# Performance work log

Measured on AMD Instinct MI355X. Metric: run time of the kernel, lower is better.

The kernel has to match this reference:

```python
import math
import jax, jax.numpy as jnp
import numpy as np

S, D = 4096, 2048
H, DH = 16, 128
ROPE_BASE = 10000.0


def _rotate_half(x):
    # x: [..., dh]; pairs (x1, x2) -> (-x2, x1), interleaved
    shp = x.shape
    x = x.reshape(*shp[:-1], shp[-1] // 2, 2)
    x1, x2 = x[..., 0], x[..., 1]
    return jnp.stack((-x2, x1), axis=-1).reshape(shp)


def _rope_cos_sin(seq_len, dh):
    inv_freq = 1.0 / (ROPE_BASE ** (jnp.arange(0, dh, 2, dtype=jnp.float32) / dh))
    t = jnp.arange(seq_len, dtype=jnp.float32)
    freqs = jnp.einsum('i,j->ij', t, inv_freq)  # [S, dh/2]
    cos = jnp.repeat(jnp.cos(freqs), 2, axis=-1)  # [S, dh]
    sin = jnp.repeat(jnp.sin(freqs), 2, axis=-1)
    return cos, sin


def setup_inputs() -> dict:
    key = jax.random.key(0)
    kx, kq, kk, kv, ko = jax.random.split(key, 5)
    scale_in = 1.0 / math.sqrt(D)
    scale_hd = 1.0 / math.sqrt(H * DH)
    return {
        'x': jax.random.normal(kx, (S, D), dtype=jnp.float32),
        'mask': jnp.tril(jnp.ones((S, S), dtype=bool)),  # causal
        'wq': jax.random.normal(kq, (H * DH, D), dtype=jnp.float32) * scale_in,
        'wk': jax.random.normal(kk, (H * DH, D), dtype=jnp.float32) * scale_in,
        'wv': jax.random.normal(kv, (H * DH, D), dtype=jnp.float32) * scale_in,
        'wo': jax.random.normal(ko, (D, H * DH), dtype=jnp.float32) * scale_hd,
    }


def reference(x, mask, wq, wk, wv, wo):
    s = x.shape[0]
    # QKV projections (Linear: y = W @ x per token) -> [h, S, dh]
    q = (x @ wq.T).reshape(s, H, DH).transpose(1, 0, 2)
    k = (x @ wk.T).reshape(s, H, DH).transpose(1, 0, 2)
    v = (x @ wv.T).reshape(s, H, DH).transpose(1, 0, 2)
    # RoPE
    cos, sin = _rope_cos_sin(s, DH)  # [S, dh] each
    q = q * cos[None] + _rotate_half(q) * sin[None]
    k = k * cos[None] + _rotate_half(k) * sin[None]
    # Attention
    sim = jnp.einsum('hid,hjd->hij', q, k) / math.sqrt(DH)  # [h, S, S]
    sim = jnp.where(mask[None], sim, -jnp.inf)
    attn = jax.nn.softmax(sim, axis=-1)
    out = jnp.einsum('hij,hjd->ihd', attn, v).reshape(s, H * DH)
    return out @ wo.T
```

## Files before the change

### kernel.cpp

```cpp
#include <hip/hip_runtime.h>
#include <stdint.h>

#define S_LEN 4096
#define D_MODEL 2048
#define NH 16
#define DH 128

typedef short s16x8 __attribute__((ext_vector_type(8)));
typedef short s16x2 __attribute__((ext_vector_type(2)));
typedef unsigned short u16;
typedef unsigned short u16x4 __attribute__((ext_vector_type(4)));
typedef float f32x4 __attribute__((ext_vector_type(4)));

__device__ __forceinline__ u16 f2bf(float f) {
  union { float f; uint32_t u; } v; v.f = f;
  uint32_t u = v.u;
  u += 0x7FFFu + ((u >> 16) & 1u);
  return (u16)(u >> 16);
}

__device__ __forceinline__ float bf2f(u16 b) {
  union { uint32_t u; float f; } v; v.u = ((uint32_t)b) << 16;
  return v.f;
}

__device__ __forceinline__ void async_copy16(const u16* g, u16* l) {
  __builtin_amdgcn_global_load_lds(
      (const __attribute__((address_space(1))) unsigned int*)g,
      (__attribute__((address_space(3))) unsigned int*)l, 16, 0, 0);
}

__global__ void cast_kernel(const float4* __restrict__ src, u16* __restrict__ dst, int n4) {
  int i = blockIdx.x * blockDim.x + threadIdx.x;
  if (i >= n4) return;
  float4 v = src[i];
  u16x4 o;
  o[0] = f2bf(v.x); o[1] = f2bf(v.y); o[2] = f2bf(v.z); o[3] = f2bf(v.w);
  *(u16x4*)(dst + (size_t)i * 4) = o;
}

__global__ void cast4_kernel(const float4* __restrict__ s0, const float4* __restrict__ s1,
                             const float4* __restrict__ s2, const float4* __restrict__ s3,
                             u16* __restrict__ d0, u16* __restrict__ d1,
                             u16* __restrict__ d2, u16* __restrict__ d3) {
  int b = blockIdx.x;
  int which = b >> 12;
  const float4* src = which == 0 ? s0 : which == 1 ? s1 : which == 2 ? s2 : s3;
  u16* dst = which == 0 ? d0 : which == 1 ? d1 : which == 2 ? d2 : d3;
  int i = (b & 4095) * blockDim.x + threadIdx.x;
  float4 v = src[i];
  u16x4 o;
  o[0] = f2bf(v.x); o[1] = f2bf(v.y); o[2] = f2bf(v.z); o[3] = f2bf(v.w);
  *(u16x4*)(dst + (size_t)i * 4) = o;
}

__global__ void rope_table(float* __restrict__ ctab, float* __restrict__ stab) {
  int idx = blockIdx.x * blockDim.x + threadIdx.x;
  int t = idx >> 6, p = idx & 63;
  float invf = powf(10000.0f, -(float)p / 64.0f);
  float th = (float)t * invf;
  ctab[idx] = cosf(th);
  stab[idx] = sinf(th);
}

#define G256_BAR() __builtin_amdgcn_s_barrier()
#define G256_LGK0() do { asm volatile("s_waitcnt lgkmcnt(0)" ::: "memory"); \
                         __builtin_amdgcn_sched_barrier(0); } while (0)
#define G256_VMC4() asm volatile("s_waitcnt vmcnt(4)" ::: "memory")

__device__ __forceinline__ void stage128(const u16* __restrict__ src, u16* dst,
                                         int rr, int gc, int ldk) {
  const u16* s = src + (size_t)rr * ldk + gc;
  u16* d = dst + (threadIdx.x << 3);
  async_copy16(s, d);
  async_copy16(s + (size_t)64 * ldk, d + 4096);
}

__device__ __forceinline__ void mma256_core(
    const u16* __restrict__ Ab,
    const u16* __restrict__ Bb,
    const int K, u16* lds, f32x4 (&acc)[8][4])
{
  const int tid = threadIdx.x;
  const int lane = tid & 63, quad = lane >> 4, l16 = lane & 15;
  const int w = tid >> 6, wr = w >> 2, wc = w & 3;
  const int rr = tid >> 3;
  const int gc = ((tid & 7) ^ (rr & 7)) << 3;

  u16* const A0b = lds;
  u16* const B0b = lds + 16384;
  u16* const A1b = lds + 32768;
  u16* const B1b = lds + 49152;

  const int NT = K >> 6;

  auto sA = [&](int t, int hh, u16* buf) {
    int tc = t < NT ? t : NT - 1;
    stage128(Ab + (size_t)(hh << 7) * K + ((size_t)tc << 6), buf + (hh << 13), rr, gc, K);
  };
  auto sB = [&](int t, int hh, u16* buf) {
    int tc = t < NT ? t : NT - 1;
    stage128(Bb + (size_t)(hh << 7) * K + ((size_t)tc << 6), buf + (hh << 13), rr, gc, K);
  };

  s16x8 a[4][2], b[4][2];
  auto rA = [&](const u16* buf, int mh) {
#pragma unroll
    for (int mt = 0; mt < 4; ++mt) {
      int ra = (wr << 7) + (mh << 6) + (mt << 4) + l16;
#pragma unroll
      for (int ks = 0; ks < 2; ++ks)
        a[mt][ks] = *(const s16x8*)(buf + (ra << 6) + ((((ks << 2) + quad) ^ (ra & 7)) << 3));
    }
  };
  auto rB = [&](const u16* buf, int nh) {
#pragma unroll
    for (int nt = 0; nt < 2; ++nt) {
      int rb = (wc << 6) + (((nh << 1) + nt) << 4) + l16;
#pragma unroll
      for (int ks = 0; ks < 2; ++ks)
        b[(nh << 1) + nt][ks] =
            *(const s16x8*)(buf + (rb << 6) + ((((ks << 2) + quad) ^ (rb & 7)) << 3));
    }
  };
  auto mmaq = [&](int mh, int nh) {
    __builtin_amdgcn_s_setprio(1);
#pragma unroll
    for (int mt = 0; mt < 4; ++mt)
#pragma unroll
      for (int nt = 0; nt < 2; ++nt) {
#pragma unroll
        for (int ks = 0; ks < 2; ++ks)
          acc[(mh << 2) + mt][(nh << 1) + nt] = __builtin_amdgcn_mfma_f32_16x16x32_bf16(
              a[mt][ks], b[(nh << 1) + nt][ks], acc[(mh << 2) + mt][(nh << 1) + nt], 0, 0, 0);
      }
    __builtin_amdgcn_s_setprio(0);
  };

  sB(0, 0, B0b); sB(0, 1, B0b); sA(0, 0, A0b); sA(0, 1, A0b);
  sB(1, 0, B1b); sB(1, 1, B1b);
  G256_VMC4();
  G256_BAR();

  const int NI = K >> 7;
#pragma unroll 1
  for (int i = 0; i < NI; ++i) {
    const int t1 = 2 * i + 1, t2 = 2 * i + 2, t3 = 2 * i + 3;
    sA(t1, 0, A1b);
    rA(A0b, 0); rB(B0b, 0);
    G256_BAR(); G256_LGK0(); mmaq(0, 0); G256_BAR();
    sA(t1, 1, A1b);
    rB(B0b, 1);
    G256_BAR(); G256_LGK0(); mmaq(0, 1); G256_BAR();
    sB(t2, 0, B0b);
    rA(A0b, 1);
    G256_BAR(); G256_LGK0(); mmaq(1, 0); G256_BAR();
    sB(t2, 1, B0b);
    G256_VMC4();
    G256_BAR(); mmaq(1, 1); G256_BAR();
    sA(t2, 0, A0b);
    rA(A1b, 0); rB(B1b, 0);
    G256_BAR(); G256_LGK0(); mmaq(0, 0); G256_BAR();
    sA(t2, 1, A0b);
    rB(B1b, 1);
    G256_BAR(); G256_LGK0(); mmaq(0, 1); G256_BAR();
    sB(t3, 0, B1b);
    rA(A1b, 1);
    G256_BAR(); G256_LGK0(); mmaq(1, 0); G256_BAR();
    sB(t3, 1, B1b);
    G256_VMC4();
    G256_BAR(); mmaq(1, 1); G256_BAR();
  }
}

__global__ __launch_bounds__(512) void gemm256_qkv(
    const u16* __restrict__ A,
    const u16* __restrict__ wqb, const u16* __restrict__ wkb, const u16* __restrict__ wvb,
    u16* __restrict__ qh, u16* __restrict__ kh, u16* __restrict__ vh,
    const float* __restrict__ ctab, const float* __restrict__ stab)
{
  __shared__ __align__(16) u16 lds[65536];
  const int tid = threadIdx.x;
  const int lane = tid & 63, quad = lane >> 4, l16 = lane & 15;
  const int w = tid >> 6, wr = w >> 2, wc = w & 3;
  const int m0 = blockIdx.x << 8;
  const int by = blockIdx.y;
  const int which = by >> 3;
  const int n0 = (by & 7) << 8;
  const u16* B = which == 0 ? wqb : which == 1 ? wkb : wvb;
  u16* outp = which == 0 ? qh : which == 1 ? kh : vh;

  f32x4 acc[8][4];
  f32x4 zero = {0.f, 0.f, 0.f, 0.f};
#pragma unroll
  for (int i = 0; i < 8; ++i)
#pragma unroll
    for (int j = 0; j < 4; ++j) acc[i][j] = zero;

  mma256_core(A + (size_t)m0 * D_MODEL, B + (size_t)n0 * D_MODEL, D_MODEL, lds, acc);

#pragma unroll
  for (int Mt = 0; Mt < 8; ++Mt) {
    int rowg = m0 + (wr << 7) + (Mt << 4) + (quad << 2);
#pragma unroll
    for (int Nt = 0; Nt < 4; ++Nt) {
      int cl = n0 + (wc << 6) + (Nt << 4) + l16;
      int hh = cl >> 7, dd = cl & 127;
      int p = dd >> 1;
      f32x4 v = acc[Mt][Nt];
#pragma unroll
      for (int r = 0; r < 4; ++r) {
        float val = v[r];
        if (which < 2) {
          float partner = __shfl_xor(val, 1);
          float c = ctab[(size_t)(rowg + r) * 64 + p];
          float s = stab[(size_t)(rowg + r) * 64 + p];
          val = (dd & 1) ? fmaf(val, c, partner * s) : fmaf(val, c, -partner * s);
        }
        outp[((size_t)hh * S_LEN + (rowg + r)) * DH + dd] = f2bf(val);
      }
    }
  }
}

__global__ __launch_bounds__(512) void gemm256_out(
    const u16* __restrict__ A, const u16* __restrict__ B, float* __restrict__ outF)
{
  __shared__ __align__(16) u16 lds[65536];
  const int tid = threadIdx.x;
  const int lane = tid & 63, quad = lane >> 4, l16 = lane & 15;
  const int w = tid >> 6, wr = w >> 2, wc = w & 3;
  const int m0 = blockIdx.x << 8, n0 = blockIdx.y << 8;

  f32x4 acc[8][4];
  f32x4 zero = {0.f, 0.f, 0.f, 0.f};
#pragma unroll
  for (int i = 0; i < 8; ++i)
#pragma unroll
    for (int j = 0; j < 4; ++j) acc[i][j] = zero;

  mma256_core(A + (size_t)m0 * D_MODEL, B + (size_t)n0 * D_MODEL, D_MODEL, lds, acc);

#pragma unroll
  for (int Mt = 0; Mt < 8; ++Mt) {
    int rowg = m0 + (wr << 7) + (Mt << 4) + (quad << 2);
#pragma unroll
    for (int Nt = 0; Nt < 4; ++Nt) {
      int col = n0 + (wc << 6) + (Nt << 4) + l16;
      f32x4 v = acc[Mt][Nt];
#pragma unroll
      for (int r = 0; r < 4; ++r) outF[(size_t)(rowg + r) * D_MODEL + col] = v[r];
    }
  }
}

__global__ __launch_bounds__(512) void attn_kernel(
    const u16* __restrict__ Q, const u16* __restrict__ Kb,
    const u16* __restrict__ V,
    u16* __restrict__ U0, u16* __restrict__ U1, float* __restrict__ lbuf)
{
  __shared__ __align__(16) u16 lk[2][64 * 128];
  __shared__ __align__(16) u16 lvt[2][128 * 64];
  __shared__ __align__(16) u16 lp[8 * 1024];

  const int tid = threadIdx.x;
  const int w = tid >> 6, lane = tid & 63, quad = lane >> 4, l16 = lane & 15;
  const int h = blockIdx.y;
  const int bx = blockIdx.x;

  const u16* Qh = Q + (size_t)h * S_LEN * DH;
  const u16* Kh = Kb + (size_t)h * S_LEN * DH;
  const u16* Vh = V + (size_t)h * S_LEN * DH;

  const float scale = 0.08838834764831845f;
  const s16x8 vones = {0x3F80, 0x3F80, 0x3F80, 0x3F80, 0x3F80, 0x3F80, 0x3F80, 0x3F80};
  f32x4 zero = {0.f, 0.f, 0.f, 0.f};
  u16* lpw = lp + (w << 10);

  for (int seg = 0; seg < 2; ++seg) {
    const int qt = seg ? bx : (31 - bx);
    const int jlo = seg ? (qt + 1) : 0;
    const int jhi = seg ? (2 * qt + 2) : (qt + 1);
    const int i0 = qt << 7;
    const int iw = i0 + (w << 4);

    s16x8 qf[4];
#pragma unroll
    for (int ks = 0; ks < 4; ++ks)
      qf[ks] = *(const s16x8*)(Qh + (size_t)(iw + l16) * DH + ks * 32 + quad * 8);

    f32x4 accO[8];
#pragma unroll
    for (int dt = 0; dt < 8; ++dt) accO[dt] = zero;
    f32x4 accL = zero;

    {
      const int j0 = jlo << 6;
      int u = tid & 31, c8 = tid >> 5, r0 = u << 1;
      s16x8 v0 = *(const s16x8*)(Vh + (size_t)(j0 + r0) * DH + (c8 << 3));
      s16x8 v1 = *(const s16x8*)(Vh + (size_t)(j0 + r0 + 1) * DH + (c8 << 3));
#pragma unroll
      for (int rnd = 0; rnd < 2; ++rnd) {
        int c = rnd * 512 + tid;
        int r = c >> 4, cc = c & 15;
        int gcol = ((cc ^ (r & 15)) << 3);
        async_copy16(Kh + (size_t)(j0 + r) * DH + gcol, lk[0] + ((rnd * 512 + w * 64) << 3));
      }
      int cc = r0 >> 3;
#pragma unroll
      for (int e = 0; e < 8; ++e) {
        int d = (c8 << 3) + e;
        int off = (d << 6) + ((cc ^ (d & 7)) << 3) + (r0 & 7);
        s16x2 pr = {v0[e], v1[e]};
        *(s16x2*)(lvt[0] + off) = pr;
      }
    }
    __syncthreads();

    int cur = 0;
    for (int jt = jlo; jt < jhi; ++jt) {
      const int j0 = jt << 6;
      const bool has_next = (jt + 1) < jhi;

      s16x8 nv0, nv1;
      if (has_next) {
        const int nj0 = (jt + 1) << 6;
        int u = tid & 31, c8 = tid >> 5, r0 = u << 1;
        nv0 = *(const s16x8*)(Vh + (size_t)(nj0 + r0) * DH + (c8 << 3));
        nv1 = *(const s16x8*)(Vh + (size_t)(nj0 + r0 + 1) * DH + (c8 << 3));
#pragma unroll
        for (int rnd = 0; rnd < 2; ++rnd) {
          int c = rnd * 512 + tid;
          int r = c >> 4, cc = c & 15;
          int gcol = ((cc ^ (r & 15)) << 3);
          async_copy16(Kh + (size_t)(nj0 + r) * DH + gcol,
                       lk[cur ^ 1] + ((rnd * 512 + w * 64) << 3));
        }
      }

      const u16* lkc = lk[cur];
      f32x4 sa[4];
#pragma unroll
      for (int nt = 0; nt < 4; ++nt) sa[nt] = zero;
      __builtin_amdgcn_s_setprio(1);
#pragma unroll
      for (int ks = 0; ks < 4; ++ks) {
#pragma unroll
        for (int nt = 0; nt < 4; ++nt) {
          int row = (nt << 4) + l16;
          s16x8 kf = *(const s16x8*)(lkc + (row << 7) + ((((ks << 2) + quad) ^ (row & 15)) << 3));
          sa[nt] = __builtin_amdgcn_mfma_f32_16x16x32_bf16(qf[ks], kf, sa[nt], 0, 0, 0);
        }
      }
      __builtin_amdgcn_s_setprio(0);

      const bool maskt = (j0 + 63 > iw);
#pragma unroll
      for (int nt = 0; nt < 4; ++nt) {
        int col = (nt << 4) + l16;
        int j = j0 + col;
        int ccp = col >> 3;
#pragma unroll
        for (int r = 0; r < 4; ++r) {
          float raw = sa[nt][r];
          if (maskt) {
            int i = iw + (quad << 2) + r;
            if (j > i) raw = -1.0e30f;
          }
          float p = __expf(fmaf(raw, scale, -8.0f));
          union { float f; uint32_t u; } pv; pv.f = p;
          int m = (quad << 2) + r;
          lpw[(m << 6) + ((ccp ^ (m & 7)) << 3) + (col & 7)] = (u16)(pv.u >> 16);
        }
      }
      asm volatile("s_waitcnt lgkmcnt(0)" ::: "memory");
      s16x8 pf[2];
#pragma unroll
      for (int kp = 0; kp < 2; ++kp)
        pf[kp] = *(const s16x8*)(lpw + (l16 << 6) + ((((kp << 2) + quad) ^ (l16 & 7)) << 3));

      if (has_next) {
        int u = tid & 31, c8 = tid >> 5, r0 = u << 1;
        int cc = r0 >> 3;
        u16* dst = lvt[cur ^ 1];
#pragma unroll
        for (int e = 0; e < 8; ++e) {
          int d = (c8 << 3) + e;
          int off = (d << 6) + ((cc ^ (d & 7)) << 3) + (r0 & 7);
          s16x2 pr = {nv0[e], nv1[e]};
          *(s16x2*)(dst + off) = pr;
        }
      }

      const u16* lvc = lvt[cur];
      __builtin_amdgcn_s_setprio(1);
      accL = __builtin_amdgcn_mfma_f32_16x16x32_bf16(pf[0], vones, accL, 0, 0, 0);
      accL = __builtin_amdgcn_mfma_f32_16x16x32_bf16(pf[1], vones, accL, 0, 0, 0);
#pragma unroll
      for (int dt = 0; dt < 8; ++dt) {
#pragma unroll
        for (int kp = 0; kp < 2; ++kp) {
          int row = (dt << 4) + l16;
          s16x8 vf = *(const s16x8*)(lvc + (row << 6) + ((((kp << 2) + quad) ^ (row & 7)) << 3));
          accO[dt] = __builtin_amdgcn_mfma_f32_16x16x32_bf16(pf[kp], vf, accO[dt], 0, 0, 0);
        }
      }
      __builtin_amdgcn_s_setprio(0);

      __syncthreads();
      cur ^= 1;
    }

    u16* Useg = seg ? U1 : U0;
    float* ls = lbuf + (size_t)seg * NH * S_LEN + (size_t)h * S_LEN;
#pragma unroll
    for (int r = 0; r < 4; ++r) {
      float lr = accL[r];
      float inv = lr > 0.f ? 1.0f / lr : 0.f;
      int srow = iw + (quad << 2) + r;
#pragma unroll
      for (int dt = 0; dt < 8; ++dt)
        Useg[((size_t)h * S_LEN + srow) * DH + (dt << 4) + l16] = f2bf(accO[dt][r] * inv);
      if (l16 == 0) ls[srow] = lr;
    }
  }
}

__global__ void combine_kernel(const u16* __restrict__ U0, const u16* __restrict__ U1,
                               const float* __restrict__ lbuf, u16* __restrict__ ob)
{
  int t = blockIdx.x * 256 + threadIdx.x;
  int d8 = t & 15;
  int h = (t >> 4) & 15;
  int s = t >> 8;
  float l0 = lbuf[(size_t)h * S_LEN + s];
  float l1 = lbuf[(size_t)(NH * S_LEN) + (size_t)h * S_LEN + s];
  float inv = 1.0f / (l0 + l1);
  float w0 = l0 * inv, w1 = l1 * inv;
  size_t base = ((size_t)h * S_LEN + s) * DH + d8 * 8;
  s16x8 u0 = *(const s16x8*)(U0 + base);
  s16x8 u1 = *(const s16x8*)(U1 + base);
  u16 o[8];
#pragma unroll
  for (int e = 0; e < 8; ++e)
    o[e] = f2bf(w0 * bf2f((u16)u0[e]) + w1 * bf2f((u16)u1[e]));
  *(s16x8*)(ob + ((size_t)s * D_MODEL + h * DH + d8 * 8)) = *(s16x8*)o;
}

extern "C" void kernel_launch(void* const* d_in, const int* in_sizes, int n_in,
                              void* d_out, int out_size, void* d_ws, size_t ws_size,
                              hipStream_t stream) {
  const float* x  = (const float*)d_in[0];
  const float* wq = (const float*)d_in[2];
  const float* wk = (const float*)d_in[3];
  const float* wv = (const float*)d_in[4];
  const float* wo = (const float*)d_in[5];
  float* out = (float*)d_out;

  char* ws = (char*)d_ws;
  u16* xb  = (u16*)(ws);
  u16* wqb = (u16*)(ws + (16ull << 20));
  u16* wkb = (u16*)(ws + (24ull << 20));
  u16* wvb = (u16*)(ws + (32ull << 20));
  u16* wob = (u16*)(ws + (40ull << 20));
  u16* qh  = (u16*)(ws + (48ull << 20));
  u16* kh  = (u16*)(ws + (64ull << 20));
  u16* vh  = (u16*)(ws + (80ull << 20));
  float* ctab = (float*)(ws + (96ull << 20));
  float* stab = (float*)(ws + (97ull << 20));
  u16* U0 = (u16*)(ws);
  u16* U1 = (u16*)(ws + (16ull << 20));
  float* lbuf = (float*)(ws + (32ull << 20));
  u16* ob = qh;

  const int nx4 = S_LEN * D_MODEL / 4;
  cast_kernel<<<nx4 / 256, 256, 0, stream>>>((const float4*)x, xb, nx4);
  cast4_kernel<<<4 * 4096, 256, 0, stream>>>(
      (const float4*)wq, (const float4*)wk, (const float4*)wv, (const float4*)wo,
      wqb, wkb, wvb, wob);
  rope_table<<<(S_LEN * 64) / 256, 256, 0, stream>>>(ctab, stab);

  gemm256_qkv<<<dim3(S_LEN / 256, 3 * D_MODEL / 256), 512, 0, stream>>>(
      xb, wqb, wkb, wvb, qh, kh, vh, ctab, stab);

  attn_kernel<<<dim3(32, NH), 512, 0, stream>>>(qh, kh, vh, U0, U1, lbuf);
  combine_kernel<<<S_LEN * NH * 16 / 256, 256, 0, stream>>>(U0, U1, lbuf, ob);

  gemm256_out<<<dim3(S_LEN / 256, D_MODEL / 256), 512, 0, stream>>>(
      ob, wob, out);
}
```

Measured before the change: 510.8 us.

## Switch projection GEMMs to 256x128 tiles with register double-buffered ping-pong schedule

Both the QKV and output projection GEMMs now use 256x128 output tiles instead of 256x256, with an 8-wave 4x2 layout and 96 KB of LDS instead of 128 KB. The main loop is restructured so that fragments for the next K-tile are loaded into a second register set while the current MFMAs run, with global staging issued mid-phase. The grid doubles, which improves wave quantization and may let more blocks fit per CU. The cost is lower arithmetic intensity per tile, more redundant A loads, and extra barriers.

```diff
diff --git a/kernel.cpp b/kernel.cpp
--- a/kernel.cpp
+++ b/kernel.cpp
@@ -63,113 +63,114 @@
   stab[idx] = sinf(th);
 }
 
-#define G256_BAR() __builtin_amdgcn_s_barrier()
-#define G256_LGK0() do { asm volatile("s_waitcnt lgkmcnt(0)" ::: "memory"); \
-                         __builtin_amdgcn_sched_barrier(0); } while (0)
-#define G256_VMC4() asm volatile("s_waitcnt vmcnt(4)" ::: "memory")
-
-__device__ __forceinline__ void stage128(const u16* __restrict__ src, u16* dst,
-                                         int rr, int gc, int ldk) {
-  const u16* s = src + (size_t)rr * ldk + gc;
-  u16* d = dst + (threadIdx.x << 3);
+#define PH_LGK0() do { asm volatile("s_waitcnt lgkmcnt(0)" ::: "memory"); \
+                       __builtin_amdgcn_sched_barrier(0); } while (0)
+
+__device__ __forceinline__ void stage16k(const u16* __restrict__ src, u16* dstbase,
+                                         const int K) {
+  const int tid = threadIdx.x;
+  int rr = tid >> 3;
+  int gc = ((tid & 7) ^ (rr & 7)) << 3;
+  const u16* s = src + (size_t)rr * K + gc;
+  u16* d = dstbase + (tid << 3);
   async_copy16(s, d);
-  async_copy16(s + (size_t)64 * ldk, d + 4096);
-}
-
-__device__ __forceinline__ void mma256_core(
-    const u16* __restrict__ Ab,
-    const u16* __restrict__ Bb,
-    const int K, u16* lds, f32x4 (&acc)[8][4])
+  async_copy16(s + (size_t)64 * K, d + 4096);
+}
+
+__device__ __forceinline__ void mma256x128(
+    const u16* __restrict__ Ab, const u16* __restrict__ Bb,
+    const int K, u16* lds, f32x4 (&acc)[4][4])
 {
   const int tid = threadIdx.x;
   const int lane = tid & 63, quad = lane >> 4, l16 = lane & 15;
-  const int w = tid >> 6, wr = w >> 2, wc = w & 3;
-  const int rr = tid >> 3;
-  const int gc = ((tid & 7) ^ (rr & 7)) << 3;
-
-  u16* const A0b = lds;
-  u16* const B0b = lds + 16384;
-  u16* const A1b = lds + 32768;
-  u16* const B1b = lds + 49152;
-
+  const int w = tid >> 6, wr = w >> 1, wc = w & 1;
+
+  u16* const A0 = lds;
+  u16* const B0 = lds + 16384;
+  u16* const A1 = lds + 24576;
+  u16* const B1 = lds + 40960;
   const int NT = K >> 6;
 
-  auto sA = [&](int t, int hh, u16* buf) {
+  auto sA = [&](int t, u16* buf) {
     int tc = t < NT ? t : NT - 1;
-    stage128(Ab + (size_t)(hh << 7) * K + ((size_t)tc << 6), buf + (hh << 13), rr, gc, K);
+    stage16k(Ab + ((size_t)tc << 6), buf, K);
+    stage16k(Ab + (size_t)128 * K + ((size_t)tc << 6), buf + 8192, K);
   };
-  auto sB = [&](int t, int hh, u16* buf) {
+  auto sB = [&](int t, u16* buf) {
     int tc = t < NT ? t : NT - 1;
-    stage128(Bb + (size_t)(hh << 7) * K + ((size_t)tc << 6), buf + (hh << 13), rr, gc, K);
+    stage16k(Bb + ((size_t)tc << 6), buf, K);
   };
 
-  s16x8 a[4][2], b[4][2];
-  auto rA = [&](const u16* buf, int mh) {
+  s16x8 aC[4][2], aN[4][2], bA[2][2], bB0[2][2], bB1[2][2];
+
+  auto rdA = [&](const u16* buf, s16x8 (&a)[4][2]) {
 #pragma unroll
     for (int mt = 0; mt < 4; ++mt) {
-      int ra = (wr << 7) + (mh << 6) + (mt << 4) + l16;
+      int ra = (wr << 6) + (mt << 4) + l16;
 #pragma unroll
       for (int ks = 0; ks < 2; ++ks)
         a[mt][ks] = *(const s16x8*)(buf + (ra << 6) + ((((ks << 2) + quad) ^ (ra & 7)) << 3));
     }
   };
-  auto rB = [&](const u16* buf, int nh) {
+  auto rdBh = [&](const u16* buf, int nh, s16x8 (&b)[2][2]) {
 #pragma unroll
     for (int nt = 0; nt < 2; ++nt) {
       int rb = (wc << 6) + (((nh << 1) + nt) << 4) + l16;
 #pragma unroll
       for (int ks = 0; ks < 2; ++ks)
-        b[(nh << 1) + nt][ks] =
-            *(const s16x8*)(buf + (rb << 6) + ((((ks << 2) + quad) ^ (rb & 7)) << 3));
+        b[nt][ks] = *(const s16x8*)(buf + (rb << 6) + ((((ks << 2) + quad) ^ (rb & 7)) << 3));
     }
   };
-  auto mmaq = [&](int mh, int nh) {
-    __builtin_amdgcn_s_setprio(1);
+  auto mmah = [&](s16x8 (&a)[4][2], s16x8 (&b)[2][2], int nh) {
 #pragma unroll
     for (int mt = 0; mt < 4; ++mt)
 #pragma unroll
-      for (int nt = 0; nt < 2; ++nt) {
+      for (int nt = 0; nt < 2; ++nt)
 #pragma unroll
         for (int ks = 0; ks < 2; ++ks)
-          acc[(mh << 2) + mt][(nh << 1) + nt] = __builtin_amdgcn_mfma_f32_16x16x32_bf16(
-              a[mt][ks], b[(nh << 1) + nt][ks], acc[(mh << 2) + mt][(nh << 1) + nt], 0, 0, 0);
-      }
-    __builtin_amdgcn_s_setprio(0);
+          acc[mt][(nh << 1) + nt] = __builtin_amdgcn_mfma_f32_16x16x32_bf16(
+              a[mt][ks], b[nt][ks], acc[mt][(nh << 1) + nt], 0, 0, 0);
   };
 
-  sB(0, 0, B0b); sB(0, 1, B0b); sA(0, 0, A0b); sA(0, 1, A0b);
-  sB(1, 0, B1b); sB(1, 1, B1b);
-  G256_VMC4();
-  G256_BAR();
+  sA(0, A0); sB(0, B0); sA(1, A1); sB(1, B1);
+  asm volatile("s_waitcnt vmcnt(6)" ::: "memory");
+  __builtin_amdgcn_s_barrier();
+  rdA(A0, aC); rdBh(B0, 0, bA); rdBh(B0, 1, bB0);
 
   const int NI = K >> 7;
 #pragma unroll 1
   for (int i = 0; i < NI; ++i) {
-    const int t1 = 2 * i + 1, t2 = 2 * i + 2, t3 = 2 * i + 3;
-    sA(t1, 0, A1b);
-    rA(A0b, 0); rB(B0b, 0);
-    G256_BAR(); G256_LGK0(); mmaq(0, 0); G256_BAR();
-    sA(t1, 1, A1b);
-    rB(B0b, 1);
-    G256_BAR(); G256_LGK0(); mmaq(0, 1); G256_BAR();
-    sB(t2, 0, B0b);
-    rA(A0b, 1);
-    G256_BAR(); G256_LGK0(); mmaq(1, 0); G256_BAR();
-    sB(t2, 1, B0b);
-    G256_VMC4();
-    G256_BAR(); mmaq(1, 1); G256_BAR();
-    sA(t2, 0, A0b);
-    rA(A1b, 0); rB(B1b, 0);
-    G256_BAR(); G256_LGK0(); mmaq(0, 0); G256_BAR();
-    sA(t2, 1, A0b);
-    rB(B1b, 1);
-    G256_BAR(); G256_LGK0(); mmaq(0, 1); G256_BAR();
-    sB(t3, 0, B1b);
-    rA(A1b, 1);
-    G256_BAR(); G256_LGK0(); mmaq(1, 0); G256_BAR();
-    sB(t3, 1, B1b);
-    G256_VMC4();
-    G256_BAR(); mmaq(1, 1); G256_BAR();
+    const int t0 = 2 * i, t1 = 2 * i + 1;
+    __builtin_amdgcn_s_barrier();
+    PH_LGK0();
+    __builtin_amdgcn_s_setprio(1);
+    mmah(aC, bA, 0);
+    __builtin_amdgcn_s_setprio(0);
+    asm volatile("s_waitcnt vmcnt(0)" ::: "memory");
+    __builtin_amdgcn_s_barrier();
+    __builtin_amdgcn_s_barrier();
+    PH_LGK0();
+    __builtin_amdgcn_s_setprio(1);
+    sA(t0 + 2, A0); sB(t0 + 2, B0);
+    rdA(A1, aN); rdBh(B1, 0, bA); rdBh(B1, 1, bB1);
+    mmah(aC, bB0, 1);
+    __builtin_amdgcn_s_setprio(0);
+    __builtin_amdgcn_s_barrier();
+    __builtin_amdgcn_s_barrier();
+    PH_LGK0();
+    __builtin_amdgcn_s_setprio(1);
+    mmah(aN, bA, 0);
+    __builtin_amdgcn_s_setprio(0);
+    asm volatile("s_waitcnt vmcnt(0)" ::: "memory");
+    __builtin_amdgcn_s_barrier();
+    __builtin_amdgcn_s_barrier();
+    PH_LGK0();
+    __builtin_amdgcn_s_setprio(1);
+    sA(t1 + 2, A1); sB(t1 + 2, B1);
+    if (i + 1 < NI) { rdA(A0, aC); rdBh(B0, 0, bA); rdBh(B0, 1, bB0); }
+    mmah(aN, bB1, 1);
+    __builtin_amdgcn_s_setprio(0);
+    __builtin_amdgcn_s_barrier();
   }
 }
 
@@ -179,35 +180,35 @@
     u16* __restrict__ qh, u16* __restrict__ kh, u16* __restrict__ vh,
     const float* __restrict__ ctab, const float* __restrict__ stab)
 {
-  __shared__ __align__(16) u16 lds[65536];
+  __shared__ __align__(16) u16 lds[49152];
   const int tid = threadIdx.x;
   const int lane = tid & 63, quad = lane >> 4, l16 = lane & 15;
-  const int w = tid >> 6, wr = w >> 2, wc = w & 3;
+  const int w = tid >> 6, wr = w >> 1, wc = w & 1;
   const int m0 = blockIdx.x << 8;
   const int by = blockIdx.y;
-  const int which = by >> 3;
-  const int n0 = (by & 7) << 8;
+  const int which = by >> 4;
+  const int n0 = (by & 15) << 7;
   const u16* B = which == 0 ? wqb : which == 1 ? wkb : wvb;
   u16* outp = which == 0 ? qh : which == 1 ? kh : vh;
 
-  f32x4 acc[8][4];
+  f32x4 acc[4][4];
   f32x4 zero = {0.f, 0.f, 0.f, 0.f};
 #pragma unroll
-  for (int i = 0; i < 8; ++i)
+  for (int i = 0; i < 4; ++i)
 #pragma unroll
     for (int j = 0; j < 4; ++j) acc[i][j] = zero;
 
-  mma256_core(A + (size_t)m0 * D_MODEL, B + (size_t)n0 * D_MODEL, D_MODEL, lds, acc);
-
-#pragma unroll
-  for (int Mt = 0; Mt < 8; ++Mt) {
-    int rowg = m0 + (wr << 7) + (Mt << 4) + (quad << 2);
-#pragma unroll
-    for (int Nt = 0; Nt < 4; ++Nt) {
-      int cl = n0 + (wc << 6) + (Nt << 4) + l16;
+  mma256x128(A + (size_t)m0 * D_MODEL, B + (size_t)n0 * D_MODEL, D_MODEL, lds, acc);
+
+#pragma unroll
+  for (int mt = 0; mt < 4; ++mt) {
+    int rowg = m0 + (wr << 6) + (mt << 4) + (quad << 2);
+#pragma unroll
+    for (int nt = 0; nt < 4; ++nt) {
+      int cl = n0 + (wc << 6) + (nt << 4) + l16;
       int hh = cl >> 7, dd = cl & 127;
       int p = dd >> 1;
-      f32x4 v = acc[Mt][Nt];
+      f32x4 v = acc[mt][nt];
 #pragma unroll
       for (int r = 0; r < 4; ++r) {
         float val = v[r];
@@ -226,28 +227,28 @@
 __global__ __launch_bounds__(512) void gemm256_out(
     const u16* __restrict__ A, const u16* __restrict__ B, float* __restrict__ outF)
 {
-  __shared__ __align__(16) u16 lds[65536];
+  __shared__ __align__(16) u16 lds[49152];
   const int tid = threadIdx.x;
   const int lane = tid & 63, quad = lane >> 4, l16 = lane & 15;
-  const int w = tid >> 6, wr = w >> 2, wc = w & 3;
-  const int m0 = blockIdx.x << 8, n0 = blockIdx.y << 8;
-
-  f32x4 acc[8][4];
+  const int w = tid >> 6, wr = w >> 1, wc = w & 1;
+  const int m0 = blockIdx.x << 8, n0 = blockIdx.y << 7;
+
+  f32x4 acc[4][4];
   f32x4 zero = {0.f, 0.f, 0.f, 0.f};
 #pragma unroll
-  for (int i = 0; i < 8; ++i)
+  for (int i = 0; i < 4; ++i)
 #pragma unroll
     for (int j = 0; j < 4; ++j) acc[i][j] = zero;
 
-  mma256_core(A + (size_t)m0 * D_MODEL, B + (size_t)n0 * D_MODEL, D_MODEL, lds, acc);
-
-#pragma unroll
-  for (int Mt = 0; Mt < 8; ++Mt) {
-    int rowg = m0 + (wr << 7) + (Mt << 4) + (quad << 2);
-#pragma unroll
-    for (int Nt = 0; Nt < 4; ++Nt) {
-      int col = n0 + (wc << 6) + (Nt << 4) + l16;
-      f32x4 v = acc[Mt][Nt];
+  mma256x128(A + (size_t)m0 * D_MODEL, B + (size_t)n0 * D_MODEL, D_MODEL, lds, acc);
+
+#pragma unroll
+  for (int mt = 0; mt < 4; ++mt) {
+    int rowg = m0 + (wr << 6) + (mt << 4) + (quad << 2);
+#pragma unroll
+    for (int nt = 0; nt < 4; ++nt) {
+      int col = n0 + (wc << 6) + (nt << 4) + l16;
+      f32x4 v = acc[mt][nt];
 #pragma unroll
       for (int r = 0; r < 4; ++r) outF[(size_t)(rowg + r) * D_MODEL + col] = v[r];
     }
@@ -480,12 +481,12 @@
       wqb, wkb, wvb, wob);
   rope_table<<<(S_LEN * 64) / 256, 256, 0, stream>>>(ctab, stab);
 
-  gemm256_qkv<<<dim3(S_LEN / 256, 3 * D_MODEL / 256), 512, 0, stream>>>(
+  gemm256_qkv<<<dim3(S_LEN / 256, 3 * D_MODEL / 128), 512, 0, stream>>>(
       xb, wqb, wkb, wvb, qh, kh, vh, ctab, stab);
 
   attn_kernel<<<dim3(32, NH), 512, 0, stream>>>(qh, kh, vh, U0, U1, lbuf);
   combine_kernel<<<S_LEN * NH * 16 / 256, 256, 0, stream>>>(U0, U1, lbuf, ob);
 
-  gemm256_out<<<dim3(S_LEN / 256, D_MODEL / 256), 512, 0, stream>>>(
+  gemm256_out<<<dim3(S_LEN / 256, D_MODEL / 128), 512, 0, stream>>>(
       ob, wob, out);
 }
```

New measurement: 481.4 us. 5.8% less time.
